# Performance work log

Measured on AMD Instinct MI355X. Metric: run time of the kernel, lower is better.

Reference implementation:

```python
import jax, jax.numpy as jnp
import numpy as np
import math

N_NODES, CHANNELS, N_ELEM, N_FEAT = 4096, 128, 10, 128
LS_IN = [0, 1, 2]          # input irreps per channel: 0e+1o+2e -> dim 9
L_OUT = [0, 1]             # keep_irrep_out = {0e, 1o}
L12_MAX = 3                # cap on intermediate coupling
SLICES = {0: (0, 1), 1: (1, 4), 2: (4, 9)}
PATHS1 = [l for l in L_OUT if l in LS_IN]
PATHS2 = [(l1, l2, lo) for l1 in LS_IN for l2 in LS_IN for lo in L_OUT if abs(l1 - l2) <= lo <= l1 + l2]
T12_KEYS = [(l1, l2, l12) for l1 in LS_IN for l2 in LS_IN for l12 in range(abs(l1 - l2), min(l1 + l2, L12_MAX) + 1)]
PATHS3 = [(k, l3, lo) for k in T12_KEYS for l3 in LS_IN for lo in L_OUT if abs(k[2] - l3) <= lo <= k[2] + l3]

def _su2_cg(j1, m1, j2, m2, j3, m3):
    if m3 != m1 + m2:
        return 0.0
    f = math.factorial
    vmin = max(-j1 + j2 + m3, -j1 + m1, 0)
    vmax = min(j2 + j3 + m1, j3 - j1 + j2, j3 + m3)
    C = math.sqrt((2 * j3 + 1) * f(j3 + j1 - j2) * f(j3 - j1 + j2) * f(j1 + j2 - j3) * f(j3 + m3) * f(j3 - m3)
                  / (f(j1 + j2 + j3 + 1) * f(j1 - m1) * f(j1 + m1) * f(j2 - m2) * f(j2 + m2)))
    S = 0.0
    for v in range(vmin, vmax + 1):
        S += (-1) ** (v + j2 + m2) * f(j2 + j3 + m1 - v) * f(j1 - m1 + v) / (
            f(v) * f(j3 - j1 + j2 - v) * f(j3 + m3 - v) * f(v + j1 - j2 - m3))
    return C * S

def _c2r(l):
    # change of basis real -> complex spherical harmonics (e3nn convention)
    q = np.zeros((2 * l + 1, 2 * l + 1), dtype=np.complex128)
    for m in range(-l, 0):
        q[l + m, l + abs(m)] = 1.0 / math.sqrt(2)
        q[l + m, l - abs(m)] = -1j / math.sqrt(2)
    q[l, l] = 1.0
    for m in range(1, l + 1):
        q[l + m, l + abs(m)] = (-1) ** m / math.sqrt(2)
        q[l + m, l - abs(m)] = 1j * (-1) ** m / math.sqrt(2)
    return (-1j) ** l * q

_CG = {}
def real_cg(l1, l2, l3):
    key = (l1, l2, l3)
    if key not in _CG:
        Cc = np.zeros((2 * l1 + 1, 2 * l2 + 1, 2 * l3 + 1), dtype=np.complex128)
        for i, m1 in enumerate(range(-l1, l1 + 1)):
            for j, m2 in enumerate(range(-l2, l2 + 1)):
                for k, m3 in enumerate(range(-l3, l3 + 1)):
                    Cc[i, j, k] = _su2_cg(l1, m1, l2, m2, l3, m3)
        R = np.einsum('ij,kl,mn,ikn->jlm', _c2r(l1), _c2r(l2), np.conj(_c2r(l3).T), Cc)
        _CG[key] = np.real(R).astype(np.float32)
    return _CG[key]

def setup_inputs():
    key = jax.random.key(0)
    k = jax.random.split(key, 8)
    node_feats = jax.random.normal(k[0], (N_NODES, CHANNELS, 9), dtype=jnp.float32)
    species = jax.random.randint(k[1], (N_NODES,), 0, N_ELEM)
    w1 = jax.random.normal(k[2], (N_ELEM, len(PATHS1), CHANNELS), dtype=jnp.float32) / math.sqrt(len(PATHS1))
    w2 = jax.random.normal(k[3], (N_ELEM, len(PATHS2), CHANNELS), dtype=jnp.float32) / math.sqrt(len(PATHS2))
    w3 = jax.random.normal(k[4], (N_ELEM, len(PATHS3), CHANNELS), dtype=jnp.float32) / math.sqrt(len(PATHS3))
    lin_w0 = jax.random.normal(k[5], (CHANNELS, N_FEAT), dtype=jnp.float32)
    lin_w1 = jax.random.normal(k[6], (CHANNELS, N_FEAT), dtype=jnp.float32)
    return {"node_feats": node_feats, "w1": w1, "w2": w2, "w3": w3,
            "lin_w0": lin_w0, "lin_w1": lin_w1, "species": species}

def reference(node_feats, w1, w2, w3, lin_w0, lin_w1, species):
    n, c = node_feats.shape[:2]
    attrs = jax.nn.one_hot(species, N_ELEM, dtype=node_feats.dtype)
    A = {l: node_feats[..., SLICES[l][0]:SLICES[l][1]] for l in LS_IN}
    # element-dependent path weights per node
    w1n = jnp.einsum('ne,epc->npc', attrs, w1)
    w2n = jnp.einsum('ne,epc->npc', attrs, w2)
    w3n = jnp.einsum('ne,epc->npc', attrs, w3)
    B = {lo: jnp.zeros((n, c, 2 * lo + 1), node_feats.dtype) for lo in L_OUT}
    # correlation order 1
    for p, lo in enumerate(PATHS1):
        B[lo] = B[lo] + w1n[:, p, :, None] * A[lo]
    for p, (l1, l2, lo) in enumerate(PATHS2):
        cg = jnp.asarray(real_cg(l1, l2, lo))
        t = jnp.einsum('ijk,nci,ncj->nck', cg, A[l1], A[l2])
        B[lo] = B[lo] + w2n[:, p, :, None] * t
    T12 = {}
    for kk in T12_KEYS:
        l1, l2, l12 = kk
        T12[kk] = jnp.einsum('ijk,nci,ncj->nck', jnp.asarray(real_cg(l1, l2, l12)), A[l1], A[l2])
    for p, (kk, l3, lo) in enumerate(PATHS3):
        cg = jnp.asarray(real_cg(kk[2], l3, lo))
        t = jnp.einsum('ijk,nci,ncj->nck', cg, T12[kk], A[l3])
        B[lo] = B[lo] + w3n[:, p, :, None] * t
    # equivariant Linear: mix channel axis into num_features per output irrep
    s = 1.0 / math.sqrt(c)
    out0 = jnp.einsum('ncm,cf->nfm', B[0], lin_w0) * s
    out1 = jnp.einsum('ncm,cf->nfm', B[1], lin_w1) * s
    return jnp.concatenate([out0, out1], axis=-1)  # [N, F, 1+3]
```

## Files before the change

kernel.cpp:

```cpp
#include <hip/hip_runtime.h>
#include <utility>


#define NN 4096
#define NC 128
#define NE 10

typedef float v2f __attribute__((ext_vector_type(2)));

__device__ __forceinline__ v2f ld2(const float* p) {
  return *reinterpret_cast<const v2f*>(p);
}
__device__ __forceinline__ v2f cfma(float c, v2f x, v2f a) {
  v2f cc = {c, c};
  return __builtin_elementwise_fma(cc, x, a);
}
__device__ __forceinline__ v2f vfma(v2f w, v2f x, v2f a) {
  return __builtin_elementwise_fma(w, x, a);
}

template<typename F, int... Is>
__device__ __forceinline__ void sfor_impl(F&& f, std::integer_sequence<int, Is...>) {
  (f(std::integral_constant<int, Is>{}), ...);
}
template<int N, typename F>
__device__ __forceinline__ void sfor(F&& f) {
  sfor_impl((F&&)f, std::make_integer_sequence<int, N>{});
}

constexpr int T_L1c[19]  = {0,0,0,1,1,1,1,1,1,1,2,2,2,2,2,2,2,2,3};
constexpr int T_L2c[19]  = {0,1,2,0,1,1,1,2,2,2,0,1,1,1,2,2,2,2,2};
constexpr int T_L3c[19]  = {0,1,2,1,0,1,2,1,2,3,2,1,2,3,0,1,2,3,1};
constexpr int T_OFFc[19] = {0,1,10,35,44,53,80,125,170,245,350,375,420,495,600,625,700,825,1000};
constexpr int AOFFc[3]   = {0,1,4};

constexpr int P2U_L1c[7]  = {0,0,1,1,1,2,2};
constexpr int P2U_L2c[7]  = {0,1,1,1,2,2,2};
constexpr int P2U_LOc[7]  = {0,1,0,1,1,0,1};
constexpr int P2U_TBLc[7] = {0,1,4,5,7,14,15};
constexpr int P2U_WAc[7]  = {0,1,3,4,5,7,8};
constexpr int P2U_WBc[7]  = {-1,2,-1,-1,6,-1,-1};

constexpr int K_L1c[18]  = {0,0,0,1,1,1,1,1,1,1,2,2,2,2,2,2,2,2};
constexpr int K_L2c[18]  = {0,1,2,0,1,1,1,2,2,2,0,1,1,1,2,2,2,2};
constexpr int K_L12c[18] = {0,1,2,1,0,1,2,1,2,3,2,1,2,3,0,1,2,3};

constexpr int   TT_CANONc[18] = {0,1,2,1,4,5,6,7,8,9,2,7,8,9,14,15,16,17};
constexpr float TT_SGNc[18]   = {1,1,1,1,1,1,1,1,1,1,1,1,-1,1,1,1,1,1};
constexpr int CANONc[13] = {0,1,2,4,5,6,7,8,9,14,15,16,17};
constexpr int CONS2c[13] = {-1,3,10,-1,-1,-1,11,12,13,-1,-1,-1,-1};

constexpr int P3_STARTc[19] = {0,2,6,9,13,15,19,22,26,29,30,33,37,40,41,43,47,50,51};
constexpr int P3_L3c[51] = {
  0,1,  0,1,1,2,  1,2,2,  0,1,1,2,  0,1,  0,1,1,2,  1,2,2,  0,1,1,2,  1,2,2,
  2,  1,2,2,  0,1,1,2,  1,2,2,  2,  0,1,  0,1,1,2,  1,2,2,  2 };
constexpr int P3_LOc[51] = {
  0,1,  1,0,1,1,  1,0,1,  1,0,1,1,  0,1,  1,0,1,1,  1,0,1,  1,0,1,1,  1,0,1,
  1,  1,0,1,  1,0,1,1,  1,0,1,  1,  0,1,  1,0,1,1,  1,0,1,  1 };
constexpr int P3_TBLc[51] = {
  0,1,  3,4,5,7,  11,14,15,  3,4,5,7,  0,1,  3,4,5,7,  11,14,15,  3,4,5,7,
  11,14,15,  18,  11,14,15,  3,4,5,7,  11,14,15,  18,  0,1,  3,4,5,7,
  11,14,15,  18 };

constexpr double cfact(int n) { double r = 1.0; for (int i = 2; i <= n; ++i) r *= i; return r; }
constexpr double csqrt(double x) {
  if (x <= 0.0) return 0.0;
  double r = x > 1.0 ? x : 1.0;
  for (int i = 0; i < 64; ++i) r = 0.5 * (r + x / r);
  return r;
}
constexpr double su2cg(int j1, int m1, int j2, int m2, int j3, int m3) {
  if (m3 != m1 + m2) return 0.0;
  int vmin = -j1 + j2 + m3; if (-j1 + m1 > vmin) vmin = -j1 + m1; if (vmin < 0) vmin = 0;
  int vmax = j2 + j3 + m1; if (j3 - j1 + j2 < vmax) vmax = j3 - j1 + j2; if (j3 + m3 < vmax) vmax = j3 + m3;
  double C = csqrt((2.0 * j3 + 1.0)
                   * cfact(j3 + j1 - j2) * cfact(j3 - j1 + j2) * cfact(j1 + j2 - j3)
                   * cfact(j3 + m3) * cfact(j3 - m3)
                   / (cfact(j1 + j2 + j3 + 1) * cfact(j1 - m1) * cfact(j1 + m1)
                      * cfact(j2 - m2) * cfact(j2 + m2)));
  double S = 0.0;
  for (int v = vmin; v <= vmax; ++v) {
    double sgn = ((v + j2 + m2) & 1) ? -1.0 : 1.0;
    S += sgn * cfact(j2 + j3 + m1 - v) * cfact(j1 - m1 + v)
         / (cfact(v) * cfact(j3 - j1 + j2 - v) * cfact(j3 + m3 - v) * cfact(v + j1 - j2 - m3));
  }
  return C * S;
}

struct Cx { double re, im; };
constexpr Cx cxmul(Cx a, Cx b) { return Cx{a.re * b.re - a.im * b.im, a.re * b.im + a.im * b.re}; }
struct Row { int cnt; int col[2]; Cx v[2]; };

constexpr Row c2r_row(int l, int r) {
  Row out{0, {0, 0}, {{0, 0}, {0, 0}}};
  constexpr double is2 = 0.70710678118654752440;
  const int m = r - l;
  if (m < 0) {
    out.cnt = 2;
    out.col[0] = l - m; out.v[0] = Cx{is2, 0.0};
    out.col[1] = l + m; out.v[1] = Cx{0.0, -is2};
  } else if (m == 0) {
    out.cnt = 1; out.col[0] = l; out.v[0] = Cx{1.0, 0.0};
  } else {
    const double sgn = (m & 1) ? -1.0 : 1.0;
    out.cnt = 2;
    out.col[0] = l + m; out.v[0] = Cx{sgn * is2, 0.0};
    out.col[1] = l - m; out.v[1] = Cx{0.0, sgn * is2};
  }
  const int ph = l & 3;
  for (int a = 0; a < out.cnt; ++a) {
    Cx v = out.v[a];
    out.v[a] = (ph == 0) ? v
             : (ph == 1) ? Cx{v.im, -v.re}
             : (ph == 2) ? Cx{-v.re, -v.im}
                         : Cx{-v.im, v.re};
  }
  return out;
}

struct CGAll { float v[1105]; };
constexpr CGAll make_cg() {
  CGAll R{};
  for (int t = 0; t < 19; ++t) {
    const int l1 = T_L1c[t], l2 = T_L2c[t], l3 = T_L3c[t], off = T_OFFc[t];
    const int d1 = 2 * l1 + 1, d2 = 2 * l2 + 1, d3 = 2 * l3 + 1;
    double tmp[175] = {};
    for (int i = 0; i < d1; ++i) {
      const int m1 = i - l1;
      const Row r1 = c2r_row(l1, i);
      for (int k = 0; k < d2; ++k) {
        const int m2 = k - l2, m3 = m1 + m2;
        if (m3 < -l3 || m3 > l3) continue;
        const double cc = su2cg(l1, m1, l2, m2, l3, m3);
        if (cc == 0.0) continue;
        const Row r2 = c2r_row(l2, k);
        const Row r3 = c2r_row(l3, m3 + l3);
        for (int a = 0; a < r1.cnt; ++a)
          for (int b = 0; b < r2.cnt; ++b) {
            const Cx q12 = cxmul(r1.v[a], r2.v[b]);
            for (int cdx = 0; cdx < r3.cnt; ++cdx) {
              const double re = q12.re * r3.v[cdx].re + q12.im * r3.v[cdx].im;
              tmp[(r1.col[a] * d2 + r2.col[b]) * d3 + r3.col[cdx]] += re * cc;
            }
          }
      }
    }
    const int sz = d1 * d2 * d3;
    for (int e = 0; e < sz; ++e) R.v[off + e] = (float)tmp[e];
  }
  return R;
}
constexpr CGAll CG_ALL = make_cg();

constexpr bool check_cg_sym() {
  for (int t = 0; t < 18; ++t) {
    const int tc = TT_CANONc[t];
    if (tc == t) continue;
    const int l1 = K_L1c[t], l2 = K_L2c[t], l12 = K_L12c[t];
    const int d1 = 2*l1+1, d2 = 2*l2+1, d12 = 2*l12+1;
    for (int i = 0; i < d1; ++i)
      for (int j = 0; j < d2; ++j)
        for (int k = 0; k < d12; ++k) {
          float a = CG_ALL.v[T_OFFc[t]  + (i*d2 + j)*d12 + k];
          float b = TT_SGNc[t] * CG_ALL.v[T_OFFc[tc] + (j*d1 + i)*d12 + k];
          float d = a - b; if (d < 0) d = -d;
          if (d > 1e-5f) return false;
        }
  }
  return true;
}
static_assert(check_cg_sym(), "CG exchange symmetry violated");

__global__ __launch_bounds__(256) void epb_fused(
    const float*  __restrict__ nf,
    const float*  __restrict__ w1,
    const float*  __restrict__ w2,
    const float*  __restrict__ w3,
    const float4* __restrict__ lw0_4,
    const float4* __restrict__ lw1_4,
    const int*    __restrict__ species,
    float* __restrict__ out)
{
  __shared__ float4 Bsh[4 * NC];
  __shared__ float4 Red[16 * NC];

  const int t  = threadIdx.x;
  const int nb = blockIdx.x * 4;

  {
    const int nl = t >> 6;
    const int c0 = (t & 63) * 2;
    const int n  = nb + nl;
    const int s  = species[n];

    const float* ap = nf + ((size_t)n * NC + c0) * 9;
    v2f A[9];
    sfor<9>([&](auto I) { A[I.value] = v2f{ap[I.value], ap[I.value + 9]}; });

    const float* w1p = w1 + (size_t)s * 2  * NC + c0;
    const float* w2p = w2 + (size_t)s * 9  * NC + c0;
    const float* w3p = w3 + (size_t)s * 51 * NC + c0;

    v2f B[4];
    {
      const v2f wa = ld2(w1p), wb = ld2(w1p + NC);
      B[0] = wa * A[0];
      B[1] = wb * A[1];
      B[2] = wb * A[2];
      B[3] = wb * A[3];
    }

    sfor<7>([&](auto P) {
      constexpr int p  = P.value;
      constexpr int l1 = P2U_L1c[p], l2 = P2U_L2c[p], lo = P2U_LOc[p];
      constexpr int d1 = 2*l1+1, d2 = 2*l2+1, dl = 2*lo+1;
      constexpr int off = T_OFFc[P2U_TBLc[p]];
      v2f w = ld2(w2p + P2U_WAc[p] * NC);
      if constexpr (P2U_WBc[p] >= 0) w = w + ld2(w2p + P2U_WBc[p] * NC);
      sfor<dl>([&](auto Kk) {
        constexpr int k = Kk.value;
        v2f v = {0.f, 0.f};
        sfor<d1>([&](auto I) {
          sfor<d2>([&](auto J) {
            constexpr float cgc = CG_ALL.v[off + (I.value * d2 + J.value) * dl + k];
            if constexpr (cgc != 0.0f) {
              constexpr int ia = AOFFc[l1] + I.value, ja = AOFFc[l2] + J.value;
              constexpr int x = ia < ja ? ia : ja, y = ia < ja ? ja : ia;
              v = cfma(cgc, A[x] * A[y], v);
            }
          });
        });
        B[lo + k] = vfma(w, v, B[lo + k]);
      });
    });

    sfor<13>([&](auto CI) {
      constexpr int tk  = CANONc[CI.value];
      constexpr int l1  = K_L1c[tk], l2 = K_L2c[tk], l12 = K_L12c[tk];
      constexpr int d1  = 2*l1+1, d2 = 2*l2+1, d12 = 2*l12+1;
      constexpr int off = T_OFFc[tk];
      v2f tt[d12];
      sfor<d12>([&](auto Kk) {
        constexpr int k = Kk.value;
        v2f v = {0.f, 0.f};
        sfor<d1>([&](auto I) {
          sfor<d2>([&](auto J) {
            constexpr float cgc = CG_ALL.v[off + (I.value * d2 + J.value) * d12 + k];
            if constexpr (cgc != 0.0f) {
              constexpr int ia = AOFFc[l1] + I.value, ja = AOFFc[l2] + J.value;
              constexpr int x = ia < ja ? ia : ja, y = ia < ja ? ja : ia;
              v = cfma(cgc, A[x] * A[y], v);
            }
          });
        });
        tt[k] = v;
      });

      auto consume = [&](auto TK, auto SG) {
        constexpr int tkey = TK.value;
        constexpr float sgn = (float)SG.value;
        constexpr int pcnt = P3_STARTc[tkey + 1] - P3_STARTc[tkey];
        sfor<pcnt>([&](auto PP) {
          constexpr int p  = P3_STARTc[tkey] + PP.value;
          constexpr int l3 = P3_L3c[p], lo = P3_LOc[p];
          constexpr int d3 = 2*l3+1, dl = 2*lo+1;
          constexpr int off2 = T_OFFc[P3_TBLc[p]];
          const v2f w = ld2(w3p + p * NC);
          sfor<dl>([&](auto M) {
            v2f v = {0.f, 0.f};
            sfor<d12>([&](auto Kk) {
              sfor<d3>([&](auto J) {
                constexpr float cgc = sgn * CG_ALL.v[off2 + (Kk.value * d3 + J.value) * dl + M.value];
                if constexpr (cgc != 0.0f)
                  v = cfma(cgc, tt[Kk.value] * A[AOFFc[l3] + J.value], v);
              });
            });
            B[lo + M.value] = vfma(w, v, B[lo + M.value]);
          });
        });
      };
      consume(std::integral_constant<int, tk>{}, std::integral_constant<int, 1>{});
      constexpr int td = CONS2c[CI.value];
      if constexpr (td >= 0)
        consume(std::integral_constant<int, td>{},
                std::integral_constant<int, (int)TT_SGNc[td]>{});
    });

    Bsh[nl * NC + c0]     = make_float4(B[0].x, B[1].x, B[2].x, B[3].x);
    Bsh[nl * NC + c0 + 1] = make_float4(B[0].y, B[1].y, B[2].y, B[3].y);
  }
  __syncthreads();

  const int q   = t & 31;
  const int dup = (t >> 5) & 1;
  const int wv  = t >> 6;
  const int n0  = dup * 2;

  float4 acc[2][4] = {};

  const float4* w0c = lw0_4 + (size_t)(wv * 32) * 32 + q;
  const float4* w1c = lw1_4 + (size_t)(wv * 32) * 32 + q;
  const float4* bp0 = &Bsh[ n0      * NC + wv * 32];
  const float4* bp1 = &Bsh[(n0 + 1) * NC + wv * 32];

  #pragma unroll 1
  for (int g = 0; g < 4; ++g) {
    float4 wA[8], wB[8];
    sfor<8>([&](auto I) {
      wA[I.value] = w0c[(size_t)(g * 8 + I.value) * 32];
      wB[I.value] = w1c[(size_t)(g * 8 + I.value) * 32];
    });
    sfor<8>([&](auto I) {
      const int i = g * 8 + I.value;
      const float4 wa = wA[I.value];
      const float4 wb = wB[I.value];
      const float4 ba = bp0[i];
      const float4 bb = bp1[i];
#define FQ(f, waf, wbf) \
      acc[0][f].x = fmaf(ba.x, waf, acc[0][f].x); \
      acc[0][f].y = fmaf(ba.y, wbf, acc[0][f].y); \
      acc[0][f].z = fmaf(ba.z, wbf, acc[0][f].z); \
      acc[0][f].w = fmaf(ba.w, wbf, acc[0][f].w); \
      acc[1][f].x = fmaf(bb.x, waf, acc[1][f].x); \
      acc[1][f].y = fmaf(bb.y, wbf, acc[1][f].y); \
      acc[1][f].z = fmaf(bb.z, wbf, acc[1][f].z); \
      acc[1][f].w = fmaf(bb.w, wbf, acc[1][f].w);
      FQ(0, wa.x, wb.x)
      FQ(1, wa.y, wb.y)
      FQ(2, wa.z, wb.z)
      FQ(3, wa.w, wb.w)
#undef FQ
    });
  }

  sfor<2>([&](auto NN_) {
    sfor<4>([&](auto F_) {
      Red[((n0 + NN_.value) * 4 + F_.value) * NC + wv * 32 + q] = acc[NN_.value][F_.value];
    });
  });
  __syncthreads();

  const float s4 = 0.08838834764831845f;
  float4* o4 = reinterpret_cast<float4*>(out);
  sfor<2>([&](auto O_) {
    const int oid = 2 * t + O_.value;
    const int n   = oid >> 7;
    const int rem = oid & 127;
    const int row = (n * 4 + (rem & 3)) * NC + (rem >> 2);
    const float4 r0 = Red[row];
    const float4 r1 = Red[row + 32];
    const float4 r2 = Red[row + 64];
    const float4 r3 = Red[row + 96];
    o4[(size_t)(nb + n) * NC + rem] = make_float4(
        ((r0.x + r1.x) + (r2.x + r3.x)) * s4,
        ((r0.y + r1.y) + (r2.y + r3.y)) * s4,
        ((r0.z + r1.z) + (r2.z + r3.z)) * s4,
        ((r0.w + r1.w) + (r2.w + r3.w)) * s4);
  });
}

extern "C" void kernel_launch(void* const* d_in, const int* in_sizes, int n_in,
                              void* d_out, int out_size, void* d_ws, size_t ws_size,
                              hipStream_t stream) {
  const float* nf  = (const float*)d_in[0];
  const float* w1  = (const float*)d_in[1];
  const float* w2  = (const float*)d_in[2];
  const float* w3  = (const float*)d_in[3];
  const float* lw0 = (const float*)d_in[4];
  const float* lw1 = (const float*)d_in[5];
  const int*   spc = (const int*)  d_in[6];
  float* out = (float*)d_out;
  (void)d_ws; (void)ws_size; (void)in_sizes; (void)n_in; (void)out_size;

  hipLaunchKernelGGL(epb_fused, dim3(NN / 4), dim3(256), 0, stream,
                     nf, w1, w2, w3, (const float4*)lw0, (const float4*)lw1,
                     spc, out);
}
```

Baseline: 98.04 us.

## Repack per-species weights into paired float4 layout and vectorize node-feature loads

Adds a pre-pass kernel that repacks w1/w2/w3 into a workspace, ordered by consumption and interleaving two paths' weights for two channels per float4. The main kernel then fetches two weights per 128-bit load instead of separate 64-bit loads. Node features are read with unaligned 4-wide vector loads instead of 18 scalar loads. This costs an extra kernel launch and the repack work on every call.

New measurement: 99.04 us. No clear change (+1.0%).

```diff
diff --git a/kernel.cpp b/kernel.cpp
--- a/kernel.cpp
+++ b/kernel.cpp
@@ -7,6 +7,7 @@
 #define NE 10
 
 typedef float v2f __attribute__((ext_vector_type(2)));
+typedef float f4u __attribute__((ext_vector_type(4), aligned(4)));
 
 __device__ __forceinline__ v2f ld2(const float* p) {
   return *reinterpret_cast<const v2f*>(p);
@@ -61,6 +62,24 @@
   0,1,  3,4,5,7,  11,14,15,  3,4,5,7,  0,1,  3,4,5,7,  11,14,15,  3,4,5,7,
   11,14,15,  18,  11,14,15,  3,4,5,7,  11,14,15,  18,  0,1,  3,4,5,7,
   11,14,15,  18 };
+
+struct PackO { int ord[62]; int pos[62]; };
+constexpr PackO make_pack() {
+  PackO P{};
+  int k = 0;
+  P.ord[k++] = 0; P.ord[k++] = 1;
+  for (int j = 0; j < 9; ++j) P.ord[k++] = 2 + j;
+  for (int ci = 0; ci < 13; ++ci) {
+    const int tk = CANONc[ci];
+    for (int p = P3_STARTc[tk]; p < P3_STARTc[tk + 1]; ++p) P.ord[k++] = 11 + p;
+    const int td = CONS2c[ci];
+    if (td >= 0)
+      for (int p = P3_STARTc[td]; p < P3_STARTc[td + 1]; ++p) P.ord[k++] = 11 + p;
+  }
+  for (int i = 0; i < 62; ++i) P.pos[P.ord[i]] = i;
+  return P;
+}
+constexpr PackO PK = make_pack();
 
 constexpr double cfact(int n) { double r = 1.0; for (int i = 2; i <= n; ++i) r *= i; return r; }
 constexpr double csqrt(double x) {
@@ -171,11 +190,30 @@
 }
 static_assert(check_cg_sym(), "CG exchange symmetry violated");
 
+__global__ __launch_bounds__(256) void epb_wt(
+    const float* __restrict__ w1,
+    const float* __restrict__ w2,
+    const float* __restrict__ w3,
+    float4* __restrict__ wt)
+{
+  const int idx = blockIdx.x * 256 + threadIdx.x;
+  if (idx >= NE * 31 * 64) return;
+  const int cp   = idx & 63;
+  const int slot = (idx >> 6) % 31;
+  const int e    = (idx >> 6) / 31;
+  const int pa = PK.ord[2 * slot], pb = PK.ord[2 * slot + 1];
+  auto src = [&](int pi, int c) -> float {
+    if (pi < 2)  return w1[((size_t)e * 2  + pi)        * NC + c];
+    if (pi < 11) return w2[((size_t)e * 9  + (pi - 2))  * NC + c];
+    return              w3[((size_t)e * 51 + (pi - 11)) * NC + c];
+  };
+  wt[idx] = make_float4(src(pa, 2 * cp),     src(pb, 2 * cp),
+                        src(pa, 2 * cp + 1), src(pb, 2 * cp + 1));
+}
+
 __global__ __launch_bounds__(256) void epb_fused(
     const float*  __restrict__ nf,
-    const float*  __restrict__ w1,
-    const float*  __restrict__ w2,
-    const float*  __restrict__ w3,
+    const float4* __restrict__ wt,
     const float4* __restrict__ lw0_4,
     const float4* __restrict__ lw1_4,
     const int*    __restrict__ species,
@@ -189,21 +227,36 @@
 
   {
     const int nl = t >> 6;
-    const int c0 = (t & 63) * 2;
+    const int cp = t & 63;
+    const int c0 = cp * 2;
     const int n  = nb + nl;
     const int s  = species[n];
 
     const float* ap = nf + ((size_t)n * NC + c0) * 9;
     v2f A[9];
-    sfor<9>([&](auto I) { A[I.value] = v2f{ap[I.value], ap[I.value + 9]}; });
-
-    const float* w1p = w1 + (size_t)s * 2  * NC + c0;
-    const float* w2p = w2 + (size_t)s * 9  * NC + c0;
-    const float* w3p = w3 + (size_t)s * 51 * NC + c0;
+    {
+      const f4u v0 = *reinterpret_cast<const f4u*>(ap);
+      const f4u v1 = *reinterpret_cast<const f4u*>(ap + 4);
+      const f4u v2 = *reinterpret_cast<const f4u*>(ap + 8);
+      const f4u v3 = *reinterpret_cast<const f4u*>(ap + 12);
+      const v2f v4 = ld2(ap + 16);
+      A[0] = v2f{v0[0], v2[1]}; A[1] = v2f{v0[1], v2[2]}; A[2] = v2f{v0[2], v2[3]};
+      A[3] = v2f{v0[3], v3[0]}; A[4] = v2f{v1[0], v3[1]}; A[5] = v2f{v1[1], v3[2]};
+      A[6] = v2f{v1[2], v3[3]}; A[7] = v2f{v1[3], v4.x};  A[8] = v2f{v2[0], v4.y};
+    }
+
+    const float4* wtp = wt + (size_t)s * 31 * 64 + cp;
+    auto getw = [&](auto PI) -> v2f {
+      constexpr int pos = PK.pos[PI.value];
+      const float4 q = wtp[(pos >> 1) * 64];
+      if constexpr (pos & 1) return v2f{q.y, q.w};
+      else                   return v2f{q.x, q.z};
+    };
 
     v2f B[4];
     {
-      const v2f wa = ld2(w1p), wb = ld2(w1p + NC);
+      const v2f wa = getw(std::integral_constant<int, 0>{});
+      const v2f wb = getw(std::integral_constant<int, 1>{});
       B[0] = wa * A[0];
       B[1] = wb * A[1];
       B[2] = wb * A[2];
@@ -215,8 +268,9 @@
       constexpr int l1 = P2U_L1c[p], l2 = P2U_L2c[p], lo = P2U_LOc[p];
       constexpr int d1 = 2*l1+1, d2 = 2*l2+1, dl = 2*lo+1;
       constexpr int off = T_OFFc[P2U_TBLc[p]];
-      v2f w = ld2(w2p + P2U_WAc[p] * NC);
-      if constexpr (P2U_WBc[p] >= 0) w = w + ld2(w2p + P2U_WBc[p] * NC);
+      v2f w = getw(std::integral_constant<int, 2 + P2U_WAc[p]>{});
+      if constexpr (P2U_WBc[p] >= 0)
+        w = w + getw(std::integral_constant<int, 2 + P2U_WBc[p]>{});
       sfor<dl>([&](auto Kk) {
         constexpr int k = Kk.value;
         v2f v = {0.f, 0.f};
@@ -265,7 +319,7 @@
           constexpr int l3 = P3_L3c[p], lo = P3_LOc[p];
           constexpr int d3 = 2*l3+1, dl = 2*lo+1;
           constexpr int off2 = T_OFFc[P3_TBLc[p]];
-          const v2f w = ld2(w3p + p * NC);
+          const v2f w = getw(std::integral_constant<int, 11 + p>{});
           sfor<dl>([&](auto M) {
             v2f v = {0.f, 0.f};
             sfor<d12>([&](auto Kk) {
@@ -370,9 +424,12 @@
   const float* lw1 = (const float*)d_in[5];
   const int*   spc = (const int*)  d_in[6];
   float* out = (float*)d_out;
-  (void)d_ws; (void)ws_size; (void)in_sizes; (void)n_in; (void)out_size;
-
+  float4* wt = (float4*)d_ws;
+  (void)ws_size; (void)in_sizes; (void)n_in; (void)out_size;
+
+  hipLaunchKernelGGL(epb_wt, dim3((NE * 31 * 64 + 255) / 256), dim3(256), 0,
+                     stream, w1, w2, w3, wt);
   hipLaunchKernelGGL(epb_fused, dim3(NN / 4), dim3(256), 0, stream,
-                     nf, w1, w2, w3, (const float4*)lw0, (const float4*)lw1,
+                     nf, wt, (const float4*)lw0, (const float4*)lw1,
                      spc, out);
 }
```
